# Kernel tuning notes

Hardware: AMD Instinct MI355X
Metric: run time of the kernel (lower is better)

Reference implementation:

```python
import jax, jax.numpy as jnp
import numpy as np

N_NODES = 100000
N_EDGES = 20000
NNZ = 1600000


def _hconv(x, node_idx, edge_idx, W, b):
    # PyG HypergraphConv (no attention): out = D^-1 H (B^-1 H^T (x W)) + b
    xw = x @ W  # [N, F_out]
    ones = jnp.ones((node_idx.shape[0],), dtype=x.dtype)
    Bdeg = jax.ops.segment_sum(ones, edge_idx, num_segments=N_EDGES)
    Binv = jnp.where(Bdeg > 0, 1.0 / Bdeg, 0.0)
    # node -> hyperedge aggregation
    e = jax.ops.segment_sum(xw[node_idx], edge_idx, num_segments=N_EDGES)
    e = e * Binv[:, None]
    Ddeg = jax.ops.segment_sum(ones, node_idx, num_segments=N_NODES)
    Dinv = jnp.where(Ddeg > 0, 1.0 / Ddeg, 0.0)
    # hyperedge -> node aggregation
    out = jax.ops.segment_sum(e[edge_idx], node_idx, num_segments=N_NODES)
    return out * Dinv[:, None] + b


def setup_inputs() -> dict:
    key = jax.random.key(0)
    ks = jax.random.split(key, 12)
    x = jax.random.normal(ks[0], (N_NODES, 300), dtype=jnp.float32)
    node_idx = jax.random.randint(ks[1], (NNZ,), 0, N_NODES)
    edge_idx = jax.random.randint(ks[2], (NNZ,), 0, N_EDGES)
    hyper_edge_index = jnp.stack([node_idx, edge_idx], axis=0)
    def lin(kw, kb, fi, fo):
        s = 1.0 / np.sqrt(fi)
        W = jax.random.uniform(kw, (fi, fo), jnp.float32, -s, s)
        b = jax.random.uniform(kb, (fo,), jnp.float32, -s, s)
        return W, b
    W1, b1 = lin(ks[3], ks[4], 300, 256)
    W2, b2 = lin(ks[5], ks[6], 256, 256)
    W3, b3 = lin(ks[7], ks[8], 256, 128)
    attn_W, attn_b = lin(ks[9], ks[10], 128, 1)
    return {"x": x, "hyper_edge_index": hyper_edge_index,
            "W1": W1, "b1": b1, "W2": W2, "b2": b2,
            "W3": W3, "b3": b3, "attn_W": attn_W, "attn_b": attn_b}


def reference(x, hyper_edge_index, W1, b1, W2, b2, W3, b3, attn_W, attn_b):
    node_idx = hyper_edge_index[0]
    edge_idx = hyper_edge_index[1]
    h = jax.nn.leaky_relu(_hconv(x, node_idx, edge_idx, W1, b1), negative_slope=0.01)
    # dropout is identity at inference
    h = jax.nn.leaky_relu(_hconv(h, node_idx, edge_idx, W2, b2), negative_slope=0.01)
    h = _hconv(h, node_idx, edge_idx, W3, b3)  # [N, 128]
    # attention pooling over all nodes (softmax along dim 0)
    logits = h @ attn_W + attn_b  # [N, 1]
    attn = jax.nn.softmax(logits, axis=0)
    return jnp.sum(attn * h, axis=0)  # [128]
```

## Files before the change

kernel.cpp:

```cpp
#include <hip/hip_runtime.h>
#include <hip/hip_bf16.h>
#include <string.h>

#define N_NODES 100000
#define N_EDGES 20000
#define NNZ     1600000

#define CHUNK   8192
#define NBE     157
#define NBN     391
#define CAP_E   11264
#define CAP_N   4864
#define NBLK_BIN ((NNZ + CHUNK - 1) / CHUNK)


__device__ __forceinline__ unsigned short f2bf(float f) {
    unsigned int u = __float_as_uint(f);
    unsigned int r = (u + 0x7fffu + ((u >> 16) & 1u)) >> 16;
    return (unsigned short)r;
}
__device__ __forceinline__ float bflo(unsigned int v) { return __uint_as_float(v << 16); }
__device__ __forceinline__ float bfhi(unsigned int v) { return __uint_as_float(v & 0xffff0000u); }
__device__ __forceinline__ unsigned int packbf(float lo, float hi) {
    return ((unsigned int)f2bf(hi) << 16) | (unsigned int)f2bf(lo);
}

__device__ __forceinline__ void async_copy16(const void* g, void* l) {
    __builtin_amdgcn_global_load_lds((const __attribute__((address_space(1))) void*)g,
                                     (__attribute__((address_space(3))) void*)l, 16, 0, 0);
}

typedef __attribute__((ext_vector_type(8))) short bf16x8;
typedef __attribute__((ext_vector_type(4))) float f32x4;


__global__ __launch_bounds__(256)
void bin_both(const int* __restrict__ node_idx, const int* __restrict__ edge_idx,
              int* __restrict__ curE, int* __restrict__ curN,
              unsigned int* __restrict__ stagedE, unsigned int* __restrict__ stagedN) {
    __shared__ int hE[NBE], gE[NBE], hN[NBN], gN[NBN];
    int t = threadIdx.x;
    for (int i = t; i < NBE; i += 256) hE[i] = 0;
    for (int i = t; i < NBN; i += 256) hN[i] = 0;
    __syncthreads();
    long base = (long)blockIdx.x * CHUNK;
    for (int k = 0; k < CHUNK / 256; k++) {
        long i = base + t + k * 256;
        if (i < NNZ) {
            atomicAdd(&hE[edge_idx[i] >> 7], 1);
            atomicAdd(&hN[node_idx[i] >> 8], 1);
        }
    }
    __syncthreads();
    for (int i = t; i < NBE; i += 256) gE[i] = hE[i] ? atomicAdd(&curE[i], hE[i]) : 0;
    for (int i = t; i < NBN; i += 256) gN[i] = hN[i] ? atomicAdd(&curN[i], hN[i]) : 0;
    __syncthreads();
    for (int i = t; i < NBE; i += 256) hE[i] = 0;
    for (int i = t; i < NBN; i += 256) hN[i] = 0;
    __syncthreads();
    for (int k = 0; k < CHUNK / 256; k++) {
        long i = base + t + k * 256;
        if (i < NNZ) {
            int e = edge_idx[i], n = node_idx[i];
            int be = e >> 7, bn = n >> 8;
            int pe = gE[be] + atomicAdd(&hE[be], 1);
            if (pe < CAP_E) stagedE[(size_t)be * CAP_E + pe] = ((unsigned)e << 17) | (unsigned)n;
            int pn = gN[bn] + atomicAdd(&hN[bn], 1);
            if (pn < CAP_N) stagedN[(size_t)bn * CAP_N + pn] = ((unsigned)n << 15) | (unsigned)e;
        }
    }
}

__global__ __launch_bounds__(256)
void build_csr2(const unsigned int* __restrict__ staged, const int* __restrict__ cnts,
                int cap, int kshift, int bshift, int nkey,
                int* __restrict__ off, int* __restrict__ endv,
                float* __restrict__ inv, int* __restrict__ csr) {
    __shared__ int cnt[256];
    __shared__ int cur[256];
    int b = blockIdx.x, t = threadIdx.x;
    int kpb = 1 << bshift;
    int key0 = b << bshift;
    unsigned int vmask = (1u << kshift) - 1u;
    int s = b * cap;
    int n = min(cnts[b], cap);
    if (t < kpb) cnt[t] = 0;
    __syncthreads();
    for (int j = t; j < n; j += 256)
        atomicAdd(&cnt[(int)(staged[s + j] >> kshift) - key0], 1);
    __syncthreads();
    int v = (t < kpb) ? cnt[t] : 0;
    cur[t] = v; __syncthreads();
    for (int st = 1; st < 256; st <<= 1) {
        int x = (t >= st) ? cur[t - st] : 0;
        __syncthreads();
        cur[t] += x;
        __syncthreads();
    }
    int excl = cur[t] - v;
    __syncthreads();
    if (t < kpb) {
        int key = key0 + t;
        if (key < nkey) {
            off[key] = s + excl;
            endv[key] = s + excl + v;
            inv[key] = (v > 0) ? 1.0f / (float)v : 0.0f;
        }
        cur[t] = excl;
    }
    __syncthreads();
    for (int j = t; j < n; j += 256) {
        unsigned int pk = staged[s + j];
        int k = (int)(pk >> kshift) - key0;
        int pos = s + atomicAdd(&cur[k], 1);
        csr[pos] = (int)(pk & vmask);
    }
}


__global__ void convert_pad_x(const float* __restrict__ x, unsigned short* __restrict__ xb) {
    int idx = blockIdx.x * 256 + threadIdx.x;
    if (idx < N_NODES * 320) {
        int r = idx / 320, k = idx - r * 320;
        xb[idx] = (k < 300) ? f2bf(x[(size_t)r * 300 + k]) : (unsigned short)0;
    }
}

__global__ void transpose_all(const float* __restrict__ W1, const float* __restrict__ W2,
                              const float* __restrict__ W3,
                              unsigned short* __restrict__ Wt1, unsigned short* __restrict__ Wt2,
                              unsigned short* __restrict__ Wt3) {
    int b = blockIdx.x;
    int t = threadIdx.x;
    if (b < 256) {
        for (int k = t; k < 320; k += 256)
            Wt1[(size_t)b * 320 + k] = (k < 300) ? f2bf(W1[(size_t)k * 256 + b]) : (unsigned short)0;
    } else if (b < 512) {
        int n = b - 256;
        Wt2[(size_t)n * 256 + t] = f2bf(W2[(size_t)t * 256 + n]);
    } else {
        int n = b - 512;
        Wt3[(size_t)n * 256 + t] = f2bf(W3[(size_t)t * 128 + n]);
    }
}


__global__ __launch_bounds__(256)
void gemm_bf16(const unsigned short* __restrict__ A,
               const unsigned short* __restrict__ Bt,
               unsigned short* __restrict__ C,
               int M, int Kp, int N) {
    __shared__ unsigned short As[128 * 32];
    __shared__ unsigned short Bs[128 * 32];
    int tid = threadIdx.x;
    int lane = tid & 63;
    int w = tid >> 6;
    int row0 = blockIdx.x * 128;
    int col0 = blockIdx.y * 128;
    int wm = w & 1, wn = w >> 1;

    f32x4 acc[4][4];
    #pragma unroll
    for (int i = 0; i < 4; i++)
        #pragma unroll
        for (int j = 0; j < 4; j++) acc[i][j] = (f32x4){0.f, 0.f, 0.f, 0.f};

    int sr = lane >> 2;
    int sc = lane & 3;

    for (int k0 = 0; k0 < Kp; k0 += 32) {
        #pragma unroll
        for (int c = 0; c < 2; c++) {
            int r = w * 32 + c * 16 + sr;
            int gr = row0 + r; if (gr >= M) gr = M - 1;
            const unsigned short* g = A + (size_t)gr * Kp + k0 + sc * 8;
            async_copy16(g, (void*)(As + (w * 32 + c * 16) * 32));
        }
        #pragma unroll
        for (int c = 0; c < 2; c++) {
            int r = w * 32 + c * 16 + sr;
            const unsigned short* g = Bt + (size_t)(col0 + r) * Kp + k0 + sc * 8;
            async_copy16(g, (void*)(Bs + (w * 32 + c * 16) * 32));
        }
        __syncthreads();

        bf16x8 a[4], b[4];
        #pragma unroll
        for (int i = 0; i < 4; i++)
            a[i] = *(const bf16x8*)(As + (wm * 64 + i * 16 + (lane & 15)) * 32 + (lane >> 4) * 8);
        #pragma unroll
        for (int j = 0; j < 4; j++)
            b[j] = *(const bf16x8*)(Bs + (wn * 64 + j * 16 + (lane & 15)) * 32 + (lane >> 4) * 8);
        #pragma unroll
        for (int i = 0; i < 4; i++)
            #pragma unroll
            for (int j = 0; j < 4; j++)
                acc[i][j] = __builtin_amdgcn_mfma_f32_16x16x32_bf16(a[i], b[j], acc[i][j], 0, 0, 0);
        __syncthreads();
    }

    int crow = (lane >> 4) * 4;
    int ccol = lane & 15;
    #pragma unroll
    for (int i = 0; i < 4; i++)
        #pragma unroll
        for (int r = 0; r < 4; r++) {
            int gr = row0 + wm * 64 + i * 16 + crow + r;
            if (gr < M) {
                #pragma unroll
                for (int j = 0; j < 4; j++) {
                    int gc = col0 + wn * 64 + j * 16 + ccol;
                    C[(size_t)gr * N + gc] = f2bf(acc[i][j][r]);
                }
            }
        }
}


#define ACC8(v)  { a[0] += bflo((v).x); a[1] += bfhi((v).x); \
                   a[2] += bflo((v).y); a[3] += bfhi((v).y); \
                   a[4] += bflo((v).z); a[5] += bfhi((v).z); \
                   a[6] += bflo((v).w); a[7] += bfhi((v).w); }

__global__ __launch_bounds__(256)
void edge_agg256(const unsigned short* __restrict__ X, const int* __restrict__ off,
                 const int* __restrict__ endv, const int* __restrict__ csr,
                 const float* __restrict__ inv, unsigned short* __restrict__ E) {
    int wv = threadIdx.x >> 6, lane = threadIdx.x & 63;
    int seg = blockIdx.x * 4 + wv;
    if (seg >= N_EDGES) return;
    int s = off[seg], t = endv[seg];
    int half = lane >> 5, l32 = lane & 31;
    const char* Xc = (const char*)X;
    unsigned lo = (unsigned)l32 << 4;
    float a[8] = {0.f, 0.f, 0.f, 0.f, 0.f, 0.f, 0.f, 0.f};
    int j = s;
    for (; j + 12 <= t; j += 12) {
        unsigned o[6];
        #pragma unroll
        for (int q = 0; q < 6; q++) o[q] = ((unsigned)csr[j + 2 * q + half] << 9) + lo;
        uint4 v[6];
        #pragma unroll
        for (int q = 0; q < 6; q++) v[q] = *(const uint4*)(Xc + o[q]);
        __builtin_amdgcn_sched_barrier(0);
        #pragma unroll
        for (int q = 0; q < 6; q++) ACC8(v[q]);
    }
    for (; j + 1 < t; j += 2) {
        uint4 v = *(const uint4*)(Xc + (((unsigned)csr[j + half] << 9) + lo));
        ACC8(v);
    }
    if (j < t && half == 0) {
        uint4 v = *(const uint4*)(Xc + (((unsigned)csr[j] << 9) + lo));
        ACC8(v);
    }
    #pragma unroll
    for (int k = 0; k < 8; k++) a[k] += __shfl_down(a[k], 32);
    if (half == 0) {
        float bi = inv[seg];
        uint4 o;
        o.x = packbf(a[0] * bi, a[1] * bi); o.y = packbf(a[2] * bi, a[3] * bi);
        o.z = packbf(a[4] * bi, a[5] * bi); o.w = packbf(a[6] * bi, a[7] * bi);
        ((uint4*)E)[(size_t)seg * 32 + l32] = o;
    }
}

__global__ __launch_bounds__(256)
void node_agg256(const unsigned short* __restrict__ Eb, const int* __restrict__ off,
                 const int* __restrict__ endv, const int* __restrict__ csr,
                 const float* __restrict__ inv, const float* __restrict__ bias,
                 unsigned short* __restrict__ outB) {
    int wv = threadIdx.x >> 6, lane = threadIdx.x & 63;
    int seg = blockIdx.x * 4 + wv;
    if (seg >= N_NODES) return;
    int s = off[seg], t = endv[seg];
    int half = lane >> 5, l32 = lane & 31;
    const char* Ec = (const char*)Eb;
    unsigned lo = (unsigned)l32 << 4;
    float a[8] = {0.f, 0.f, 0.f, 0.f, 0.f, 0.f, 0.f, 0.f};
    int j = s;
    for (; j + 12 <= t; j += 12) {
        unsigned o[6];
        #pragma unroll
        for (int q = 0; q < 6; q++) o[q] = ((unsigned)csr[j + 2 * q + half] << 9) + lo;
        uint4 v[6];
        #pragma unroll
        for (int q = 0; q < 6; q++) v[q] = *(const uint4*)(Ec + o[q]);
        __builtin_amdgcn_sched_barrier(0);
        #pragma unroll
        for (int q = 0; q < 6; q++) ACC8(v[q]);
    }
    for (; j + 1 < t; j += 2) {
        uint4 v = *(const uint4*)(Ec + (((unsigned)csr[j + half] << 9) + lo));
        ACC8(v);
    }
    if (j < t && half == 0) {
        uint4 v = *(const uint4*)(Ec + (((unsigned)csr[j] << 9) + lo));
        ACC8(v);
    }
    #pragma unroll
    for (int k = 0; k < 8; k++) a[k] += __shfl_down(a[k], 32);
    if (half == 0) {
        float di = inv[seg];
        float4 b0 = ((const float4*)bias)[l32 * 2];
        float4 b1 = ((const float4*)bias)[l32 * 2 + 1];
        float o0 = a[0] * di + b0.x, o1 = a[1] * di + b0.y;
        float o2 = a[2] * di + b0.z, o3 = a[3] * di + b0.w;
        float o4 = a[4] * di + b1.x, o5 = a[5] * di + b1.y;
        float o6 = a[6] * di + b1.z, o7 = a[7] * di + b1.w;
        o0 = (o0 > 0.f) ? o0 : 0.01f * o0;  o1 = (o1 > 0.f) ? o1 : 0.01f * o1;
        o2 = (o2 > 0.f) ? o2 : 0.01f * o2;  o3 = (o3 > 0.f) ? o3 : 0.01f * o3;
        o4 = (o4 > 0.f) ? o4 : 0.01f * o4;  o5 = (o5 > 0.f) ? o5 : 0.01f * o5;
        o6 = (o6 > 0.f) ? o6 : 0.01f * o6;  o7 = (o7 > 0.f) ? o7 : 0.01f * o7;
        uint4 o;
        o.x = packbf(o0, o1); o.y = packbf(o2, o3);
        o.z = packbf(o4, o5); o.w = packbf(o6, o7);
        ((uint4*)outB)[(size_t)seg * 32 + l32] = o;
    }
}

__global__ __launch_bounds__(256)
void node_agg128f(const unsigned short* __restrict__ Eb, const int* __restrict__ off,
                  const int* __restrict__ endv, const int* __restrict__ csr,
                  const float* __restrict__ inv, const float* __restrict__ bias,
                  float* __restrict__ outF) {
    int wv = threadIdx.x >> 6, lane = threadIdx.x & 63;
    int seg = blockIdx.x * 4 + wv;
    if (seg >= N_NODES) return;
    int s = off[seg], t = endv[seg];
    int quad = lane >> 4, l16 = lane & 15;
    const char* Ec = (const char*)Eb;
    unsigned lo = (unsigned)l16 << 4;
    float a[8] = {0.f, 0.f, 0.f, 0.f, 0.f, 0.f, 0.f, 0.f};
    int j = s;
    for (; j + 16 <= t; j += 16) {
        unsigned o[4];
        #pragma unroll
        for (int q = 0; q < 4; q++) o[q] = ((unsigned)csr[j + 4 * q + quad] << 8) + lo;
        uint4 v[4];
        #pragma unroll
        for (int q = 0; q < 4; q++) v[q] = *(const uint4*)(Ec + o[q]);
        __builtin_amdgcn_sched_barrier(0);
        #pragma unroll
        for (int q = 0; q < 4; q++) ACC8(v[q]);
    }
    for (; j + 4 <= t; j += 4) {
        uint4 v = *(const uint4*)(Ec + (((unsigned)csr[j + quad] << 8) + lo));
        ACC8(v);
    }
    if (j < t && j + quad < t) {
        uint4 v = *(const uint4*)(Ec + (((unsigned)csr[j + quad] << 8) + lo));
        ACC8(v);
    }
    #pragma unroll
    for (int k = 0; k < 8; k++) {
        a[k] += __shfl_down(a[k], 32);
        a[k] += __shfl_down(a[k], 16);
    }
    if (lane < 16) {
        float di = inv[seg];
        float4 b0 = ((const float4*)bias)[l16 * 2];
        float4 b1 = ((const float4*)bias)[l16 * 2 + 1];
        float4 o0 = make_float4(a[0] * di + b0.x, a[1] * di + b0.y,
                                a[2] * di + b0.z, a[3] * di + b0.w);
        float4 o1 = make_float4(a[4] * di + b1.x, a[5] * di + b1.y,
                                a[6] * di + b1.z, a[7] * di + b1.w);
        ((float4*)outF)[(size_t)seg * 32 + l16 * 2]     = o0;
        ((float4*)outF)[(size_t)seg * 32 + l16 * 2 + 1] = o1;
    }
}


__global__ __launch_bounds__(256)
void logits_kernel(const float* __restrict__ H, const float* __restrict__ aW,
                   const float* __restrict__ aB, float* __restrict__ logits,
                   float* __restrict__ pmax, int N) {
    int lane = threadIdx.x & 63;
    int wave = threadIdx.x >> 6;
    int waveGlobal = blockIdx.x * 4 + wave;
    int stride = gridDim.x * 4;
    float2 w2 = ((const float2*)aW)[lane];
    float lmax = -1e30f;
    float ab = aB[0];
    for (int n = waveGlobal; n < N; n += stride) {
        float2 h2 = ((const float2*)(H + (size_t)n * 128))[lane];
        float d = h2.x * w2.x + h2.y * w2.y;
        #pragma unroll
        for (int s = 32; s > 0; s >>= 1) d += __shfl_xor(d, s, 64);
        float lg = d + ab;
        if (lane == 0) logits[n] = lg;
        lmax = fmaxf(lmax, lg);
    }
    __shared__ float wmax[4];
    if (lane == 0) wmax[wave] = lmax;
    __syncthreads();
    if (threadIdx.x == 0) {
        float m = fmaxf(fmaxf(wmax[0], wmax[1]), fmaxf(wmax[2], wmax[3]));
        pmax[blockIdx.x] = m;
    }
}

__global__ __launch_bounds__(256)
void reduce_max(const float* __restrict__ pmax, int n, float* __restrict__ gmax) {
    __shared__ float sm[256];
    float m = -1e30f;
    for (int i = threadIdx.x; i < n; i += 256) m = fmaxf(m, pmax[i]);
    sm[threadIdx.x] = m;
    __syncthreads();
    for (int s = 128; s > 0; s >>= 1) {
        if (threadIdx.x < (unsigned)s) sm[threadIdx.x] = fmaxf(sm[threadIdx.x], sm[threadIdx.x + s]);
        __syncthreads();
    }
    if (threadIdx.x == 0) *gmax = sm[0];
}

__global__ __launch_bounds__(128)
void weighted_sum(const float* __restrict__ H, const float* __restrict__ logits,
                  const float* __restrict__ gmax, float* __restrict__ gacc,
                  float* __restrict__ gsum, int N) {
    int f = threadIdx.x;
    float mx = *gmax;
    float acc = 0.f, ls = 0.f;
    for (int n = blockIdx.x; n < N; n += gridDim.x) {
        float w = __expf(logits[n] - mx);
        acc += w * H[(size_t)n * 128 + f];
        if (f == 0) ls += w;
    }
    atomicAdd(&gacc[f], acc);
    if (f == 0) atomicAdd(gsum, ls);
}

__global__ __launch_bounds__(128)
void finalize(const float* __restrict__ gacc, const float* __restrict__ gsum,
              float* __restrict__ out) {
    int f = threadIdx.x;
    out[f] = gacc[f] / gsum[0];
}


extern "C" void kernel_launch(void* const* d_in, const int* in_sizes, int n_in,
                              void* d_out, int out_size, void* d_ws, size_t ws_size,
                              hipStream_t stream) {
    const float* x        = (const float*)d_in[0];
    const int*   node_idx = (const int*)d_in[1];
    const int*   edge_idx = node_idx + NNZ;
    const float* W1 = (const float*)d_in[2];
    const float* b1 = (const float*)d_in[3];
    const float* W2 = (const float*)d_in[4];
    const float* b2 = (const float*)d_in[5];
    const float* W3 = (const float*)d_in[6];
    const float* b3 = (const float*)d_in[7];
    const float* aW = (const float*)d_in[8];
    const float* aB = (const float*)d_in[9];
    float* out = (float*)d_out;

    char* ws = (char*)d_ws;
    size_t off = 0;
    auto take = [&](size_t bytes) -> char* {
        char* r = ws + off;
        off = (off + bytes + 255) & ~(size_t)255;
        return r;
    };

    char* cur_base = take((size_t)(NBE + NBN) * 4);
    int* curE = (int*)cur_base;
    int* curN = curE + NBE;
    int*   offE = (int*)take((size_t)N_EDGES * 4);
    int*   endE = (int*)take((size_t)N_EDGES * 4);
    int*   offN = (int*)take((size_t)N_NODES * 4);
    int*   endN = (int*)take((size_t)N_NODES * 4);
    float* Binv = (float*)take((size_t)N_EDGES * 4);
    float* Dinv = (float*)take((size_t)N_NODES * 4);
    int*   csrE = (int*)take((size_t)NBE * CAP_E * 4);
    int*   csrN = (int*)take((size_t)NBN * CAP_N * 4);

    unsigned short* xb  = (unsigned short*)take((size_t)N_NODES * 320 * 2);
    unsigned short* Wt1 = (unsigned short*)take((size_t)256 * 320 * 2);
    unsigned short* Wt2 = (unsigned short*)take((size_t)256 * 256 * 2);
    unsigned short* Wt3 = (unsigned short*)take((size_t)128 * 256 * 2);
    unsigned short* xw   = (unsigned short*)take((size_t)N_NODES * 256 * 2);
    unsigned short* hb   = (unsigned short*)take((size_t)N_NODES * 256 * 2);
    unsigned short* eagg = (unsigned short*)take((size_t)N_EDGES * 256 * 2);
    unsigned short* eb   = (unsigned short*)take((size_t)N_EDGES * 256 * 2);
    float* h3 = (float*)xb;

    unsigned int* stagedE = (unsigned int*)xw;
    unsigned int* stagedN = stagedE + (size_t)NBE * CAP_E;

    float* logits = (float*)take((size_t)N_NODES * 4);
    float* pmax   = (float*)take(400 * 4);
    char* acc_base = take((128 + 1) * 4);
    float* gacc = (float*)acc_base;
    float* gsum = gacc + 128;
    float* gmax = (float*)take(4);

    hipMemsetAsync(cur_base, 0, (size_t)(NBE + NBN) * 4, stream);
    hipMemsetAsync(acc_base, 0, (128 + 1) * 4, stream);

    bin_both<<<NBLK_BIN, 256, 0, stream>>>(node_idx, edge_idx, curE, curN, stagedE, stagedN);
    build_csr2<<<NBE, 256, 0, stream>>>(stagedE, curE, CAP_E, 17, 7, N_EDGES, offE, endE, Binv, csrE);
    build_csr2<<<NBN, 256, 0, stream>>>(stagedN, curN, CAP_N, 15, 8, N_NODES, offN, endN, Dinv, csrN);

    convert_pad_x<<<(N_NODES * 320 + 255) / 256, 256, 0, stream>>>(x, xb);
    transpose_all<<<640, 256, 0, stream>>>(W1, W2, W3, Wt1, Wt2, Wt3);

    const int MB = (N_NODES + 127) / 128;
    const int ME = (N_EDGES + 127) / 128;
    const int EB = N_EDGES / 4;
    const int NB = N_NODES / 4;

    gemm_bf16<<<dim3(MB, 2), 256, 0, stream>>>(xb, Wt1, xw, N_NODES, 320, 256);
    edge_agg256<<<EB, 256, 0, stream>>>(xw, offE, endE, csrE, Binv, eb);
    node_agg256<<<NB, 256, 0, stream>>>(eb, offN, endN, csrN, Dinv, b1, hb);

    edge_agg256<<<EB, 256, 0, stream>>>(hb, offE, endE, csrE, Binv, eagg);
    gemm_bf16<<<dim3(ME, 2), 256, 0, stream>>>(eagg, Wt2, eb, N_EDGES, 256, 256);
    node_agg256<<<NB, 256, 0, stream>>>(eb, offN, endN, csrN, Dinv, b2, hb);

    edge_agg256<<<EB, 256, 0, stream>>>(hb, offE, endE, csrE, Binv, eagg);
    gemm_bf16<<<dim3(ME, 1), 256, 0, stream>>>(eagg, Wt3, eb, N_EDGES, 256, 128);
    node_agg128f<<<NB, 256, 0, stream>>>(eb, offN, endN, csrN, Dinv, b3, h3);

    logits_kernel<<<400, 256, 0, stream>>>(h3, aW, aB, logits, pmax, N_NODES);
    reduce_max<<<1, 256, 0, stream>>>(pmax, 400, gmax);
    weighted_sum<<<512, 128, 0, stream>>>(h3, logits, gmax, gacc, gsum, N_NODES);
    finalize<<<1, 128, 0, stream>>>(gacc, gsum, out);
}
```

Measured before the change: 1.028 ms.

## Vectorize x conversion, fold max reduction into weighted sum, nontemporal gather loads

Replaces the per-element x-to-bf16 conversion with a kernel where each thread reads 8 floats as float4 and writes a 16-byte packed bf16 chunk. Removes the single-block reduce_max launch; each weighted_sum block now reduces the 400 partial maxima itself. Adds a variant of the second-layer edge aggregation that gathers with nontemporal loads, meant to keep the gathered rows from displacing other data in cache. These are three separate tweaks that each trade a little redundant or cache-hint behaviour for fewer launches and wider memory accesses.

Result: no change. 1.036 ms (+0.8%).

```diff
diff --git a/kernel.cpp b/kernel.cpp
--- a/kernel.cpp
+++ b/kernel.cpp
@@ -32,6 +32,11 @@
 
 typedef __attribute__((ext_vector_type(8))) short bf16x8;
 typedef __attribute__((ext_vector_type(4))) float f32x4;
+typedef __attribute__((ext_vector_type(4))) unsigned int u32x4;
+
+__device__ __forceinline__ u32x4 ntload4(const void* p) {
+    return __builtin_nontemporal_load((const u32x4*)p);
+}
 
 
 __global__ __launch_bounds__(256)
@@ -118,12 +123,28 @@
 }
 
 
-__global__ void convert_pad_x(const float* __restrict__ x, unsigned short* __restrict__ xb) {
-    int idx = blockIdx.x * 256 + threadIdx.x;
-    if (idx < N_NODES * 320) {
-        int r = idx / 320, k = idx - r * 320;
-        xb[idx] = (k < 300) ? f2bf(x[(size_t)r * 300 + k]) : (unsigned short)0;
-    }
+__global__ __launch_bounds__(256)
+void convert_pad_x_v(const float* __restrict__ x, unsigned short* __restrict__ xb) {
+    int t = threadIdx.x;
+    if (t >= 240) return;
+    int c = t % 40;
+    int r = blockIdx.x * 6 + t / 40;
+    if (r >= N_NODES) return;
+    const float* xr = x + (size_t)r * 300 + c * 8;
+    uint4 ov;
+    if (c < 37) {
+        float4 a = ((const float4*)xr)[0];
+        float4 b = ((const float4*)xr)[1];
+        ov.x = packbf(a.x, a.y); ov.y = packbf(a.z, a.w);
+        ov.z = packbf(b.x, b.y); ov.w = packbf(b.z, b.w);
+    } else if (c == 37) {
+        float4 a = ((const float4*)xr)[0];
+        ov.x = packbf(a.x, a.y); ov.y = packbf(a.z, a.w);
+        ov.z = 0u; ov.w = 0u;
+    } else {
+        ov.x = ov.y = ov.z = ov.w = 0u;
+    }
+    *(uint4*)(xb + (size_t)r * 320 + c * 8) = ov;
 }
 
 __global__ void transpose_all(const float* __restrict__ W1, const float* __restrict__ W2,
@@ -252,6 +273,49 @@
     }
     if (j < t && half == 0) {
         uint4 v = *(const uint4*)(Xc + (((unsigned)csr[j] << 9) + lo));
+        ACC8(v);
+    }
+    #pragma unroll
+    for (int k = 0; k < 8; k++) a[k] += __shfl_down(a[k], 32);
+    if (half == 0) {
+        float bi = inv[seg];
+        uint4 o;
+        o.x = packbf(a[0] * bi, a[1] * bi); o.y = packbf(a[2] * bi, a[3] * bi);
+        o.z = packbf(a[4] * bi, a[5] * bi); o.w = packbf(a[6] * bi, a[7] * bi);
+        ((uint4*)E)[(size_t)seg * 32 + l32] = o;
+    }
+}
+
+__global__ __launch_bounds__(256)
+void edge_agg256_nt(const unsigned short* __restrict__ X, const int* __restrict__ off,
+                    const int* __restrict__ endv, const int* __restrict__ csr,
+                    const float* __restrict__ inv, unsigned short* __restrict__ E) {
+    int wv = threadIdx.x >> 6, lane = threadIdx.x & 63;
+    int seg = blockIdx.x * 4 + wv;
+    if (seg >= N_EDGES) return;
+    int s = off[seg], t = endv[seg];
+    int half = lane >> 5, l32 = lane & 31;
+    const char* Xc = (const char*)X;
+    unsigned lo = (unsigned)l32 << 4;
+    float a[8] = {0.f, 0.f, 0.f, 0.f, 0.f, 0.f, 0.f, 0.f};
+    int j = s;
+    for (; j + 12 <= t; j += 12) {
+        unsigned o[6];
+        #pragma unroll
+        for (int q = 0; q < 6; q++) o[q] = ((unsigned)csr[j + 2 * q + half] << 9) + lo;
+        u32x4 v[6];
+        #pragma unroll
+        for (int q = 0; q < 6; q++) v[q] = ntload4(Xc + o[q]);
+        __builtin_amdgcn_sched_barrier(0);
+        #pragma unroll
+        for (int q = 0; q < 6; q++) ACC8(v[q]);
+    }
+    for (; j + 1 < t; j += 2) {
+        u32x4 v = ntload4(Xc + (((unsigned)csr[j + half] << 9) + lo));
+        ACC8(v);
+    }
+    if (j < t && half == 0) {
+        u32x4 v = ntload4(Xc + (((unsigned)csr[j] << 9) + lo));
         ACC8(v);
     }
     #pragma unroll
@@ -400,26 +464,19 @@
     }
 }
 
-__global__ __launch_bounds__(256)
-void reduce_max(const float* __restrict__ pmax, int n, float* __restrict__ gmax) {
-    __shared__ float sm[256];
-    float m = -1e30f;
-    for (int i = threadIdx.x; i < n; i += 256) m = fmaxf(m, pmax[i]);
-    sm[threadIdx.x] = m;
-    __syncthreads();
-    for (int s = 128; s > 0; s >>= 1) {
-        if (threadIdx.x < (unsigned)s) sm[threadIdx.x] = fmaxf(sm[threadIdx.x], sm[threadIdx.x + s]);
-        __syncthreads();
-    }
-    if (threadIdx.x == 0) *gmax = sm[0];
-}
-
 __global__ __launch_bounds__(128)
 void weighted_sum(const float* __restrict__ H, const float* __restrict__ logits,
-                  const float* __restrict__ gmax, float* __restrict__ gacc,
+                  const float* __restrict__ pmax, float* __restrict__ gacc,
                   float* __restrict__ gsum, int N) {
     int f = threadIdx.x;
-    float mx = *gmax;
+    __shared__ float smax[2];
+    float m = -1e30f;
+    for (int i = f; i < 400; i += 128) m = fmaxf(m, pmax[i]);
+    #pragma unroll
+    for (int s = 32; s > 0; s >>= 1) m = fmaxf(m, __shfl_xor(m, s, 64));
+    if ((f & 63) == 0) smax[f >> 6] = m;
+    __syncthreads();
+    float mx = fmaxf(smax[0], smax[1]);
     float acc = 0.f, ls = 0.f;
     for (int n = blockIdx.x; n < N; n += gridDim.x) {
         float w = __expf(logits[n] - mx);
@@ -492,7 +549,6 @@
     char* acc_base = take((128 + 1) * 4);
     float* gacc = (float*)acc_base;
     float* gsum = gacc + 128;
-    float* gmax = (float*)take(4);
 
     hipMemsetAsync(cur_base, 0, (size_t)(NBE + NBN) * 4, stream);
     hipMemsetAsync(acc_base, 0, (128 + 1) * 4, stream);
@@ -501,7 +557,7 @@
     build_csr2<<<NBE, 256, 0, stream>>>(stagedE, curE, CAP_E, 17, 7, N_EDGES, offE, endE, Binv, csrE);
     build_csr2<<<NBN, 256, 0, stream>>>(stagedN, curN, CAP_N, 15, 8, N_NODES, offN, endN, Dinv, csrN);
 
-    convert_pad_x<<<(N_NODES * 320 + 255) / 256, 256, 0, stream>>>(x, xb);
+    convert_pad_x_v<<<(N_NODES + 5) / 6, 256, 0, stream>>>(x, xb);
     transpose_all<<<640, 256, 0, stream>>>(W1, W2, W3, Wt1, Wt2, Wt3);
 
     const int MB = (N_NODES + 127) / 128;
@@ -513,7 +569,7 @@
     edge_agg256<<<EB, 256, 0, stream>>>(xw, offE, endE, csrE, Binv, eb);
     node_agg256<<<NB, 256, 0, stream>>>(eb, offN, endN, csrN, Dinv, b1, hb);
 
-    edge_agg256<<<EB, 256, 0, stream>>>(hb, offE, endE, csrE, Binv, eagg);
+    edge_agg256_nt<<<EB, 256, 0, stream>>>(hb, offE, endE, csrE, Binv, eagg);
     gemm_bf16<<<dim3(ME, 2), 256, 0, stream>>>(eagg, Wt2, eb, N_EDGES, 256, 256);
     node_agg256<<<NB, 256, 0, stream>>>(eb, offN, endN, csrN, Dinv, b2, hb);
 
@@ -522,7 +578,6 @@
     node_agg128f<<<NB, 256, 0, stream>>>(eb, offN, endN, csrN, Dinv, b3, h3);
 
     logits_kernel<<<400, 256, 0, stream>>>(h3, aW, aB, logits, pmax, N_NODES);
-    reduce_max<<<1, 256, 0, stream>>>(pmax, 400, gmax);
-    weighted_sum<<<512, 128, 0, stream>>>(h3, logits, gmax, gacc, gsum, N_NODES);
+    weighted_sum<<<512, 128, 0, stream>>>(h3, logits, pmax, gacc, gsum, N_NODES);
     finalize<<<1, 128, 0, stream>>>(gacc, gsum, out);
 }
```
